# Kernel tuning notes

Measured on AMD Instinct MI355X. Metric: run time of the kernel, lower is better.

## Reference

```python
import jax, jax.numpy as jnp
import numpy as np

# e3nn normalize2mom constants: 1/sqrt(E[act(z)^2]) for z ~ N(0,1)
_z = np.random.default_rng(0).standard_normal(1_000_000)
_C_SILU = np.float32(1.0 / np.sqrt(np.mean((_z / (1.0 + np.exp(-_z))) ** 2)))
_C_SIGMOID = np.float32(1.0 / np.sqrt(np.mean((1.0 / (1.0 + np.exp(-_z))) ** 2)))

E = 131072
MUL0, MUL1 = 256, 128          # node irreps: 256x0e + 128x1e
RBF = 64
W_NUMEL = 256 + 256 + 128 + 128  # uvu weights in instruction order: A,C,B,D
INV_SQRT3 = np.float32(1.0 / np.sqrt(3.0))
INV_SQRT2 = np.float32(1.0 / np.sqrt(2.0))
INV_SQRT_FAN = np.float32(1.0 / np.sqrt(384.0))  # LinearRS rescale (fan_in=384)


def setup_inputs() -> dict:
    key = jax.random.key(0)
    ks = jax.random.split(key, 8)
    f32 = jnp.float32
    return {
        "node_input": jax.random.normal(ks[0], (E, MUL0 + MUL1 * 3), f32),
        "edge_attr": jax.random.normal(ks[1], (E, 4), f32),        # sh: 1x0e + 1x1e
        "edge_scalars": jax.random.normal(ks[2], (E, RBF), f32),
        "rad_w1": jax.random.normal(ks[3], (RBF, 64), f32) / np.float32(np.sqrt(RBF)),
        "rad_ln_g": jnp.ones((64,), f32),
        "rad_ln_b": jnp.zeros((64,), f32),
        "rad_w2": jax.random.normal(ks[4], (64, W_NUMEL), f32) / np.float32(8.0),
        "rad_offset": jnp.zeros((W_NUMEL,), f32),
        "lin_w0": jax.random.normal(ks[5], (384, 384), f32),
        "lin_b0": jnp.zeros((384,), f32),
        "lin_w1": jax.random.normal(ks[6], (384, MUL1), f32),
    }


def reference(node_input, edge_attr, edge_scalars, rad_w1, rad_ln_g, rad_ln_b,
              rad_w2, rad_offset, lin_w0, lin_b0, lin_w1):
    # --- RadialProfile: Linear(no bias) -> LayerNorm -> SiLU -> Linear(no bias) + offset
    h = edge_scalars @ rad_w1
    mu = jnp.mean(h, axis=-1, keepdims=True)
    var = jnp.var(h, axis=-1, keepdims=True)
    h = (h - mu) * jax.lax.rsqrt(var + 1e-5) * rad_ln_g + rad_ln_b
    h = jax.nn.silu(h)
    w = h @ rad_w2 + rad_offset                        # [E, 768] per-edge DTP weights
    wA, wC, wB, wD = w[:, :256], w[:, 256:512], w[:, 512:640], w[:, 640:]

    x0 = node_input[:, :MUL0]                          # [E,256]  0e
    x1 = node_input[:, MUL0:].reshape(-1, MUL1, 3)     # [E,128,3] 1e
    sh0 = edge_attr[:, 0:1]                            # [E,1]
    sh1 = edge_attr[:, 1:4]                            # [E,3]

    # --- DepthwiseTensorProduct ('uvu', path_weight = sqrt(dim(ir_out)), w3j orthonormal)
    outA = x0 * sh0 * wA                                                # 0e x 0e -> 0e [E,256]
    outB = jnp.einsum('eui,ei->eu', x1, sh1) * INV_SQRT3 * wB           # 1e . 1e -> 0e [E,128]
    outC = (x0 * wC)[:, :, None] * sh1[:, None, :]                      # 0e x 1e -> 1e [E,256,3]
    outD = jnp.cross(x1, sh1[:, None, :]) * INV_SQRT2 * wD[:, :, None]  # 1e x 1e -> 1e [E,128,3]

    d0 = jnp.concatenate([outA, outB], axis=-1)        # [E,384]   0e block (sorted irreps)
    d1 = jnp.concatenate([outC, outD], axis=1)         # [E,384,3] 1e block

    # --- LinearRS: per-irrep linear with 1/sqrt(fan_in) rescale; bias on 0e only
    out0 = d0 @ lin_w0 * INV_SQRT_FAN + lin_b0                       # [E,384] = 256 scalars + 128 gates
    out1 = jnp.einsum('eum,uv->evm', d1, lin_w1) * INV_SQRT_FAN      # [E,128,3] gated 1e

    # --- Gate: normalize2mom(SiLU) on scalars, normalize2mom(sigmoid) gates on 1e
    scalars = _C_SILU * jax.nn.silu(out0[:, :MUL0])
    gates = _C_SIGMOID * jax.nn.sigmoid(out0[:, MUL0:])
    gated = out1 * gates[:, :, None]
    return jnp.concatenate([scalars, gated.reshape(gated.shape[0], -1)], axis=-1)  # [E,640]
```

## Files before the change

### kernel.cpp

```cpp
#include <hip/hip_runtime.h>
#include <stdint.h>

typedef __attribute__((ext_vector_type(8))) short short8;
typedef __attribute__((ext_vector_type(4))) float f32x4;
typedef __attribute__((ext_vector_type(8))) float float8;

#define OW1R  0
#define OW2R  4096
#define OW0T  53248
#define OW1CT 200704
#define OW1DT 233472

#define OATTR 0
#define OES   512
#define OHS   4608
#define OD0   8704
#define OH    8704
#define OZC   33280
#define OZD0  49664
#define SMEM_BYTES 74240

static constexpr float C_SILU      = 1.6765390f;
static constexpr float C_SIG       = 1.8462240f;
static constexpr float INV_SQRT3   = 0.5773502691896258f;
static constexpr float INV_SQRT2   = 0.7071067811865476f;
static constexpr float INV_SQRT_FAN= 0.051031036307982884f;

__device__ __forceinline__ short f2bf(float f) {
  union { float f; uint32_t u; } v; v.f = f;
  uint32_t u = v.u;
  u += 0x7FFFu + ((u >> 16) & 1u);
  return (short)(u >> 16);
}

__device__ __forceinline__ f32x4 mfma16(short8 a, short8 b, f32x4 c) {
  return __builtin_amdgcn_mfma_f32_16x16x32_bf16(a, b, c, 0, 0, 0);
}

__device__ __forceinline__ short8 ldF(const short* __restrict__ W, int nkt, int nt, int kt, int lane) {
  return *(const short8*)(W + ((((nt * nkt) + kt) << 6) + lane) * 8);
}

__global__ void prep_weights(const float* __restrict__ rw1, const float* __restrict__ rw2,
                             const float* __restrict__ lw0, const float* __restrict__ lw1,
                             short* __restrict__ ws)
{
  int idx = blockIdx.x * blockDim.x + threadIdx.x;
  int stride = gridDim.x * blockDim.x;
  for (int i = idx; i < 4096; i += stride) {
    int e = i & 7, lane = (i >> 3) & 63, f = i >> 9;
    int kt = f & 1, nt = f >> 1;
    int n = nt * 16 + (lane & 15), k = kt * 32 + ((lane >> 4) << 3) + e;
    ws[OW1R + i] = f2bf(rw1[k * 64 + n]);
  }
  for (int i = idx; i < 49152; i += stride) {
    int e = i & 7, lane = (i >> 3) & 63, f = i >> 9;
    int kt = f & 1, nt = f >> 1;
    int n = nt * 16 + (lane & 15), k = kt * 32 + ((lane >> 4) << 3) + e;
    ws[OW2R + i] = f2bf(rw2[k * 768 + n]);
  }
  for (int i = idx; i < 147456; i += stride) {
    int e = i & 7, lane = (i >> 3) & 63, f = i >> 9;
    int kt = f % 12, nt = f / 12;
    int n = nt * 16 + (lane & 15), k = kt * 32 + ((lane >> 4) << 3) + e;
    ws[OW0T + i] = f2bf(lw0[k * 384 + n] * INV_SQRT_FAN);
  }
  for (int i = idx; i < 32768; i += stride) {
    int e = i & 7, lane = (i >> 3) & 63, f = i >> 9;
    int kt = f & 7, nt = f >> 3;
    int n = nt * 16 + (lane & 15), k = kt * 32 + ((lane >> 4) << 3) + e;
    ws[OW1CT + i] = f2bf(lw1[k * 128 + n] * INV_SQRT_FAN);
  }
  for (int i = idx; i < 16384; i += stride) {
    int e = i & 7, lane = (i >> 3) & 63, f = i >> 9;
    int kt = f & 3, nt = f >> 2;
    int n = nt * 16 + (lane & 15), k = kt * 32 + ((lane >> 4) << 3) + e;
    ws[OW1DT + i] = f2bf(lw1[(256 + k) * 128 + n] * INV_SQRT_FAN);
  }
}

#define SWZ(row, byte) ((byte) ^ ((((row) & 7) << 4) ^ (((row) & 8) << 2)))
#define LDA(base, c2, row, k0) \
  (*(const short8*)(smem + (base) + (row) * (c2) + SWZ(row, (k0) << 1)))
#define STBF(base, c2, row, col, val) \
  (*(short*)(smem + (base) + (row) * (c2) + SWZ(row, (col) << 1)) = f2bf(val))

__global__ __launch_bounds__(256) void fctp_fused(
    const float* __restrict__ node, const float* __restrict__ eattr,
    const float* __restrict__ escal, const float* __restrict__ lng,
    const float* __restrict__ lnb, const float* __restrict__ roff,
    const float* __restrict__ b0v, const short* __restrict__ ws,
    float* __restrict__ out)
{
  __shared__ char smem[SMEM_BYTES];
  const int t = threadIdx.x;
  const int lane = t & 63;
  const int w = t >> 6;
  const int row0 = blockIdx.x << 5;
  const int l15 = lane & 15;
  const int kof = (lane >> 4) << 3;
  const int rb0 = (lane >> 4) << 2;

  const int pr = t >> 3, pc0 = (t & 7) << 3;

  float4 lg0 = *(const float4*)(lng + pc0);
  float4 lg1 = *(const float4*)(lng + pc0 + 4);
  float4 lb0 = *(const float4*)(lnb + pc0);
  float4 lb1 = *(const float4*)(lnb + pc0 + 4);

  float offAr[4], offCr[4], offBr[2], offDr[2];
#pragma unroll
  for (int j = 0; j < 4; ++j) {
    int u = (((w << 2) + j) << 4) + l15;
    offAr[j] = roff[u];
    offCr[j] = roff[256 + u];
  }
#pragma unroll
  for (int j = 0; j < 2; ++j) {
    int u = (((w << 1) + j) << 4) + l15;
    offBr[j] = roff[512 + u];
    offDr[j] = roff[640 + u];
  }

  float s0r[2][4], sar[2][4], sbr[2][4], scr[2][4];
#pragma unroll
  for (int rt = 0; rt < 2; ++rt)
#pragma unroll
    for (int i = 0; i < 4; ++i) {
      int row = rt * 16 + rb0 + i;
      float4 att = *(const float4*)(eattr + (size_t)(row0 + row) * 4);
      s0r[rt][i] = att.x;
      sar[rt][i] = att.y;
      sbr[rt][i] = att.z;
      scr[rt][i] = att.w;
    }

  float x0r[4][2][4];
#pragma unroll
  for (int j = 0; j < 4; ++j) {
    int u = (((w << 2) + j) << 4) + l15;
#pragma unroll
    for (int rt = 0; rt < 2; ++rt)
#pragma unroll
      for (int i = 0; i < 4; ++i)
        x0r[j][rt][i] = node[(size_t)(row0 + rt * 16 + rb0 + i) * 640 + u];
  }
  float x1r[2][2][4][3];
#pragma unroll
  for (int j = 0; j < 2; ++j) {
    int u = (((w << 1) + j) << 4) + l15;
#pragma unroll
    for (int rt = 0; rt < 2; ++rt)
#pragma unroll
      for (int i = 0; i < 4; ++i) {
        const float* xp = node + (size_t)(row0 + rt * 16 + rb0 + i) * 640 + 256 + u * 3;
        x1r[j][rt][i][0] = xp[0];
        x1r[j][rt][i][1] = xp[1];
        x1r[j][rt][i][2] = xp[2];
      }
  }

  {
    short8 bf0 = ldF(ws + OW1R, 2, w, 0, lane);
    short8 bf1 = ldF(ws + OW1R, 2, w, 1, lane);
    float* sh_h = (float*)(smem + OH);
    int colh = (w << 4) + l15;
#pragma unroll
    for (int rt = 0; rt < 2; ++rt) {
      int r = rt * 16 + l15;
      const float* ep = escal + (size_t)(row0 + r) * 64;
      float8 e0 = *(const float8*)(ep + kof);
      float8 e1 = *(const float8*)(ep + 32 + kof);
      short8 ae0, ae1;
#pragma unroll
      for (int jj = 0; jj < 8; ++jj) { ae0[jj] = f2bf(e0[jj]); ae1[jj] = f2bf(e1[jj]); }
      f32x4 acc = {0.f, 0.f, 0.f, 0.f};
      acc = mfma16(ae0, bf0, acc);
      acc = mfma16(ae1, bf1, acc);
      int rb = rt * 16 + rb0;
#pragma unroll
      for (int i = 0; i < 4; ++i) sh_h[(rb + i) * 68 + colh] = acc[i];
    }
  }
  __syncthreads();

  {
    const float* sh_h = (const float*)(smem + OH);
    float vals[8]; float s = 0.f, s2 = 0.f;
#pragma unroll
    for (int j = 0; j < 8; ++j) {
      float v = sh_h[pr * 68 + pc0 + j];
      vals[j] = v; s += v; s2 += v * v;
    }
#pragma unroll
    for (int off = 1; off < 8; off <<= 1) {
      s  += __shfl_xor(s, off, 64);
      s2 += __shfl_xor(s2, off, 64);
    }
    float mu = s * 0.015625f;
    float var = s2 * 0.015625f - mu * mu;
    float rstd = rsqrtf(var + 1e-5f);
    float lg[8] = {lg0.x, lg0.y, lg0.z, lg0.w, lg1.x, lg1.y, lg1.z, lg1.w};
    float lb[8] = {lb0.x, lb0.y, lb0.z, lb0.w, lb1.x, lb1.y, lb1.z, lb1.w};
    short8 hv;
#pragma unroll
    for (int j = 0; j < 8; ++j) {
      float v = (vals[j] - mu) * rstd * lg[j] + lb[j];
      float sv = v / (1.f + __expf(-v));
      hv[j] = f2bf(sv);
    }
    *(short8*)(smem + OHS + pr * 128 + SWZ(pr, pc0 << 1)) = hv;
  }
  __syncthreads();

  {
    short8 a00 = LDA(OHS, 128, l15, kof);
    short8 a01 = LDA(OHS, 128, l15, 32 + kof);
    short8 a10 = LDA(OHS, 128, 16 + l15, kof);
    short8 a11 = LDA(OHS, 128, 16 + l15, 32 + kof);

#pragma unroll
    for (int j = 0; j < 4; ++j) {
      int ut = (w << 2) + j;
      short8 bA0 = ldF(ws + OW2R, 2, ut, 0, lane);
      short8 bA1 = ldF(ws + OW2R, 2, ut, 1, lane);
      short8 bC0 = ldF(ws + OW2R, 2, ut + 16, 0, lane);
      short8 bC1 = ldF(ws + OW2R, 2, ut + 16, 1, lane);
      int u = (ut << 4) + l15;
#pragma unroll
      for (int rt = 0; rt < 2; ++rt) {
        short8 fa = rt ? a10 : a00, fb = rt ? a11 : a01;
        f32x4 accA = {0.f,0.f,0.f,0.f}, accC = {0.f,0.f,0.f,0.f};
        accA = mfma16(fa, bA0, accA); accA = mfma16(fb, bA1, accA);
        accC = mfma16(fa, bC0, accC); accC = mfma16(fb, bC1, accC);
#pragma unroll
        for (int i = 0; i < 4; ++i) {
          int row = rt * 16 + rb0 + i;
          float x0v = x0r[j][rt][i];
          STBF(OD0, 768, row, u, x0v * s0r[rt][i] * (accA[i] + offAr[j]));
          STBF(OZC, 512, row, u, x0v * (accC[i] + offCr[j]));
        }
      }
    }
#pragma unroll
    for (int j = 0; j < 2; ++j) {
      int ut = (w << 1) + j;
      short8 bB0 = ldF(ws + OW2R, 2, 32 + ut, 0, lane);
      short8 bB1 = ldF(ws + OW2R, 2, 32 + ut, 1, lane);
      short8 bD0 = ldF(ws + OW2R, 2, 40 + ut, 0, lane);
      short8 bD1 = ldF(ws + OW2R, 2, 40 + ut, 1, lane);
      int u = (ut << 4) + l15;
#pragma unroll
      for (int rt = 0; rt < 2; ++rt) {
        short8 fa = rt ? a10 : a00, fb = rt ? a11 : a01;
        f32x4 accB = {0.f,0.f,0.f,0.f}, accD = {0.f,0.f,0.f,0.f};
        accB = mfma16(fa, bB0, accB); accB = mfma16(fb, bB1, accB);
        accD = mfma16(fa, bD0, accD); accD = mfma16(fb, bD1, accD);
#pragma unroll
        for (int i = 0; i < 4; ++i) {
          int row = rt * 16 + rb0 + i;
          float xa = x1r[j][rt][i][0], xb = x1r[j][rt][i][1], xc = x1r[j][rt][i][2];
          float sa = sar[rt][i], sb = sbr[rt][i], sc = scr[rt][i];
          float wB = accB[i] + offBr[j], wD = accD[i] + offDr[j];
          STBF(OD0, 768, row, 256 + u,
               (xa * sa + xb * sb + xc * sc) * INV_SQRT3 * wB);
          float zd = wD * INV_SQRT2;
          STBF(OZD0,          256, row, u, xa * zd);
          STBF(OZD0 + 8192,   256, row, u, xb * zd);
          STBF(OZD0 + 16384,  256, row, u, xc * zd);
        }
      }
    }
  }
  __syncthreads();


#pragma unroll
  for (int cp = 0; cp < 2; ++cp) {
    f32x4 sacc[2][2];
#pragma unroll
    for (int q = 0; q < 2; ++q)
#pragma unroll
      for (int rt = 0; rt < 2; ++rt) sacc[q][rt] = (f32x4){0.f, 0.f, 0.f, 0.f};
#pragma unroll
    for (int kt = 0; kt < 12; ++kt) {
      int k0 = kt * 32 + kof;
      short8 Af0 = LDA(OD0, 768, l15, k0);
      short8 Af1 = LDA(OD0, 768, 16 + l15, k0);
      short8 Bf0 = ldF(ws + OW0T, 12, (w << 2) + 2 * cp,     kt, lane);
      short8 Bf1 = ldF(ws + OW0T, 12, (w << 2) + 2 * cp + 1, kt, lane);
      sacc[0][0] = mfma16(Af0, Bf0, sacc[0][0]);
      sacc[0][1] = mfma16(Af1, Bf0, sacc[0][1]);
      sacc[1][0] = mfma16(Af0, Bf1, sacc[1][0]);
      sacc[1][1] = mfma16(Af1, Bf1, sacc[1][1]);
    }
#pragma unroll
    for (int q = 0; q < 2; ++q) {
      int col = (((w << 2) + 2 * cp + q) << 4) + l15;
      float bias = b0v[col];
#pragma unroll
      for (int rt = 0; rt < 2; ++rt) {
#pragma unroll
        for (int i = 0; i < 4; ++i) {
          float v = sacc[q][rt][i] + bias;
          float sv = v / (1.f + __expf(-v));
          out[(size_t)(row0 + rt * 16 + rb0 + i) * 640 + col] = C_SILU * sv;
        }
      }
    }
  }

  f32x4 gacc[2][2];
#pragma unroll
  for (int j = 0; j < 2; ++j)
#pragma unroll
    for (int rt = 0; rt < 2; ++rt) gacc[j][rt] = (f32x4){0.f, 0.f, 0.f, 0.f};
#pragma unroll
  for (int kt = 0; kt < 12; ++kt) {
    int k0 = kt * 32 + kof;
    short8 Af0 = LDA(OD0, 768, l15, k0);
    short8 Af1 = LDA(OD0, 768, 16 + l15, k0);
    short8 Bg0 = ldF(ws + OW0T, 12, 16 + (w << 1),     kt, lane);
    short8 Bg1 = ldF(ws + OW0T, 12, 16 + (w << 1) + 1, kt, lane);
    gacc[0][0] = mfma16(Af0, Bg0, gacc[0][0]);
    gacc[0][1] = mfma16(Af1, Bg0, gacc[0][1]);
    gacc[1][0] = mfma16(Af0, Bg1, gacc[1][0]);
    gacc[1][1] = mfma16(Af1, Bg1, gacc[1][1]);
  }

  f32x4 ycacc[2][2];
#pragma unroll
  for (int j = 0; j < 2; ++j)
#pragma unroll
    for (int rt = 0; rt < 2; ++rt) ycacc[j][rt] = (f32x4){0.f, 0.f, 0.f, 0.f};
  {
    short8 Az[2][8];
#pragma unroll
    for (int kt = 0; kt < 8; ++kt) {
      int k0 = kt * 32 + kof;
      Az[0][kt] = LDA(OZC, 512, l15, k0);
      Az[1][kt] = LDA(OZC, 512, 16 + l15, k0);
    }
#pragma unroll
    for (int j = 0; j < 2; ++j) {
      int vt = (w << 1) + j;
      short8 Bfr[8];
#pragma unroll
      for (int kt = 0; kt < 8; ++kt) Bfr[kt] = ldF(ws + OW1CT, 8, vt, kt, lane);
#pragma unroll
      for (int kt = 0; kt < 8; ++kt) {
        ycacc[j][0] = mfma16(Az[0][kt], Bfr[kt], ycacc[j][0]);
        ycacc[j][1] = mfma16(Az[1][kt], Bfr[kt], ycacc[j][1]);
      }
    }
  }

  f32x4 pacc[3][2][2];
#pragma unroll
  for (int m = 0; m < 3; ++m)
#pragma unroll
    for (int j = 0; j < 2; ++j)
#pragma unroll
      for (int rt = 0; rt < 2; ++rt) pacc[m][j][rt] = (f32x4){0.f, 0.f, 0.f, 0.f};
#pragma unroll
  for (int m = 0; m < 3; ++m) {
    short8 Az[2][4];
#pragma unroll
    for (int kt4 = 0; kt4 < 4; ++kt4) {
      int k0 = kt4 * 32 + kof;
      Az[0][kt4] = LDA(OZD0 + m * 8192, 256, l15, k0);
      Az[1][kt4] = LDA(OZD0 + m * 8192, 256, 16 + l15, k0);
    }
#pragma unroll
    for (int j = 0; j < 2; ++j) {
      int vt = (w << 1) + j;
      short8 Bfr[4];
#pragma unroll
      for (int kt4 = 0; kt4 < 4; ++kt4) Bfr[kt4] = ldF(ws + OW1DT, 4, vt, kt4, lane);
#pragma unroll
      for (int kt4 = 0; kt4 < 4; ++kt4) {
        pacc[m][j][0] = mfma16(Az[0][kt4], Bfr[kt4], pacc[m][j][0]);
        pacc[m][j][1] = mfma16(Az[1][kt4], Bfr[kt4], pacc[m][j][1]);
      }
    }
  }

  {
#pragma unroll
    for (int j = 0; j < 2; ++j) {
      int v = (((w << 1) + j) << 4) + l15;
      float bias = b0v[256 + v];
#pragma unroll
      for (int rt = 0; rt < 2; ++rt) {
#pragma unroll
        for (int i = 0; i < 4; ++i) {
          int row = rt * 16 + rb0 + i;
          float gate = C_SIG / (1.f + __expf(-(gacc[j][rt][i] + bias)));
          float ra = sar[rt][i], rb = sbr[rt][i], rc = scr[rt][i];
          float yc = ycacc[j][rt][i];
          float q0 = pacc[0][j][rt][i], q1 = pacc[1][j][rt][i], q2 = pacc[2][j][rt][i];
          float o0 = ra * yc + (rc * q1 - rb * q2);
          float o1 = rb * yc + (ra * q2 - rc * q0);
          float o2 = rc * yc + (rb * q0 - ra * q1);
          float* op = out + (size_t)(row0 + row) * 640 + 256 + v * 3;
          op[0] = o0 * gate; op[1] = o1 * gate; op[2] = o2 * gate;
        }
      }
    }
  }
}

extern "C" void kernel_launch(void* const* d_in, const int* in_sizes, int n_in,
                              void* d_out, int out_size, void* d_ws, size_t ws_size,
                              hipStream_t stream) {
  const float* node_input   = (const float*)d_in[0];
  const float* edge_attr    = (const float*)d_in[1];
  const float* edge_scalars = (const float*)d_in[2];
  const float* rad_w1       = (const float*)d_in[3];
  const float* rad_ln_g     = (const float*)d_in[4];
  const float* rad_ln_b     = (const float*)d_in[5];
  const float* rad_w2       = (const float*)d_in[6];
  const float* rad_offset   = (const float*)d_in[7];
  const float* lin_w0       = (const float*)d_in[8];
  const float* lin_b0       = (const float*)d_in[9];
  const float* lin_w1       = (const float*)d_in[10];
  short* wsb = (short*)d_ws;
  float* out = (float*)d_out;

  prep_weights<<<256, 256, 0, stream>>>(rad_w1, rad_w2, lin_w0, lin_w1, wsb);
  fctp_fused<<<131072 / 32, 256, 0, stream>>>(node_input, edge_attr, edge_scalars,
                                              rad_ln_g, rad_ln_b, rad_offset,
                                              lin_b0, wsb, out);
}
```

Measured before the change: 297.1 us.

## Split radial first layer and LayerNorm into a separate kernel

Moves the first radial linear layer, LayerNorm and SiLU out of the fused kernel into a new kernel that writes bf16 hidden activations to workspace. The main kernel then loads those activations straight from global memory into MFMA fragments. This drops two __syncthreads and the first-layer work from the main kernel, which may ease register pressure and shorten its critical path. The cost is an extra launch plus a round trip of roughly 16 MB of bf16 activations through global memory.

```diff
diff --git a/kernel.cpp b/kernel.cpp
--- a/kernel.cpp
+++ b/kernel.cpp
@@ -10,12 +10,9 @@
 #define OW0T  53248
 #define OW1CT 200704
 #define OW1DT 233472
-
-#define OATTR 0
-#define OES   512
-#define OHS   4608
+#define OHSG  249856
+
 #define OD0   8704
-#define OH    8704
 #define OZC   33280
 #define OZD0  49664
 #define SMEM_BYTES 74240
@@ -85,11 +82,81 @@
 #define STBF(base, c2, row, col, val) \
   (*(short*)(smem + (base) + (row) * (c2) + SWZ(row, (col) << 1)) = f2bf(val))
 
+__global__ __launch_bounds__(256) void hs_kernel(
+    const float* __restrict__ escal, const float* __restrict__ lng,
+    const float* __restrict__ lnb, const short* __restrict__ ws,
+    short* __restrict__ hsg)
+{
+  __shared__ float sh_h[32 * 68];
+  const int t = threadIdx.x;
+  const int lane = t & 63;
+  const int w = t >> 6;
+  const int row0 = blockIdx.x << 5;
+  const int l15 = lane & 15;
+  const int kof = (lane >> 4) << 3;
+  const int rb0 = (lane >> 4) << 2;
+  const int pr = t >> 3, pc0 = (t & 7) << 3;
+
+  float4 lg0 = *(const float4*)(lng + pc0);
+  float4 lg1 = *(const float4*)(lng + pc0 + 4);
+  float4 lb0 = *(const float4*)(lnb + pc0);
+  float4 lb1 = *(const float4*)(lnb + pc0 + 4);
+
+  {
+    short8 bf0 = ldF(ws + OW1R, 2, w, 0, lane);
+    short8 bf1 = ldF(ws + OW1R, 2, w, 1, lane);
+    int colh = (w << 4) + l15;
+#pragma unroll
+    for (int rt = 0; rt < 2; ++rt) {
+      int r = rt * 16 + l15;
+      const float* ep = escal + (size_t)(row0 + r) * 64;
+      float8 e0 = *(const float8*)(ep + kof);
+      float8 e1 = *(const float8*)(ep + 32 + kof);
+      short8 ae0, ae1;
+#pragma unroll
+      for (int jj = 0; jj < 8; ++jj) { ae0[jj] = f2bf(e0[jj]); ae1[jj] = f2bf(e1[jj]); }
+      f32x4 acc = {0.f, 0.f, 0.f, 0.f};
+      acc = mfma16(ae0, bf0, acc);
+      acc = mfma16(ae1, bf1, acc);
+      int rb = rt * 16 + rb0;
+#pragma unroll
+      for (int i = 0; i < 4; ++i) sh_h[(rb + i) * 68 + colh] = acc[i];
+    }
+  }
+  __syncthreads();
+
+  {
+    float vals[8]; float s = 0.f, s2 = 0.f;
+#pragma unroll
+    for (int j = 0; j < 8; ++j) {
+      float v = sh_h[pr * 68 + pc0 + j];
+      vals[j] = v; s += v; s2 += v * v;
+    }
+#pragma unroll
+    for (int off = 1; off < 8; off <<= 1) {
+      s  += __shfl_xor(s, off, 64);
+      s2 += __shfl_xor(s2, off, 64);
+    }
+    float mu = s * 0.015625f;
+    float var = s2 * 0.015625f - mu * mu;
+    float rstd = rsqrtf(var + 1e-5f);
+    float lg[8] = {lg0.x, lg0.y, lg0.z, lg0.w, lg1.x, lg1.y, lg1.z, lg1.w};
+    float lb[8] = {lb0.x, lb0.y, lb0.z, lb0.w, lb1.x, lb1.y, lb1.z, lb1.w};
+    short8 hv;
+#pragma unroll
+    for (int j = 0; j < 8; ++j) {
+      float v = (vals[j] - mu) * rstd * lg[j] + lb[j];
+      float sv = v / (1.f + __expf(-v));
+      hv[j] = f2bf(sv);
+    }
+    *(short8*)(hsg + (size_t)(row0 + pr) * 64 + pc0) = hv;
+  }
+}
+
 __global__ __launch_bounds__(256) void fctp_fused(
     const float* __restrict__ node, const float* __restrict__ eattr,
-    const float* __restrict__ escal, const float* __restrict__ lng,
-    const float* __restrict__ lnb, const float* __restrict__ roff,
-    const float* __restrict__ b0v, const short* __restrict__ ws,
+    const float* __restrict__ roff, const float* __restrict__ b0v,
+    const short* __restrict__ ws, const short* __restrict__ hsg,
     float* __restrict__ out)
 {
   __shared__ char smem[SMEM_BYTES];
@@ -101,13 +168,6 @@
   const int kof = (lane >> 4) << 3;
   const int rb0 = (lane >> 4) << 2;
 
-  const int pr = t >> 3, pc0 = (t & 7) << 3;
-
-  float4 lg0 = *(const float4*)(lng + pc0);
-  float4 lg1 = *(const float4*)(lng + pc0 + 4);
-  float4 lb0 = *(const float4*)(lnb + pc0);
-  float4 lb1 = *(const float4*)(lnb + pc0 + 4);
-
   float offAr[4], offCr[4], offBr[2], offDr[2];
 #pragma unroll
   for (int j = 0; j < 4; ++j) {
@@ -160,65 +220,12 @@
       }
   }
 
+  short8 a00 = *(const short8*)(hsg + (size_t)(row0 + l15) * 64 + kof);
+  short8 a01 = *(const short8*)(hsg + (size_t)(row0 + l15) * 64 + 32 + kof);
+  short8 a10 = *(const short8*)(hsg + (size_t)(row0 + 16 + l15) * 64 + kof);
+  short8 a11 = *(const short8*)(hsg + (size_t)(row0 + 16 + l15) * 64 + 32 + kof);
+
   {
-    short8 bf0 = ldF(ws + OW1R, 2, w, 0, lane);
-    short8 bf1 = ldF(ws + OW1R, 2, w, 1, lane);
-    float* sh_h = (float*)(smem + OH);
-    int colh = (w << 4) + l15;
-#pragma unroll
-    for (int rt = 0; rt < 2; ++rt) {
-      int r = rt * 16 + l15;
-      const float* ep = escal + (size_t)(row0 + r) * 64;
-      float8 e0 = *(const float8*)(ep + kof);
-      float8 e1 = *(const float8*)(ep + 32 + kof);
-      short8 ae0, ae1;
-#pragma unroll
-      for (int jj = 0; jj < 8; ++jj) { ae0[jj] = f2bf(e0[jj]); ae1[jj] = f2bf(e1[jj]); }
-      f32x4 acc = {0.f, 0.f, 0.f, 0.f};
-      acc = mfma16(ae0, bf0, acc);
-      acc = mfma16(ae1, bf1, acc);
-      int rb = rt * 16 + rb0;
-#pragma unroll
-      for (int i = 0; i < 4; ++i) sh_h[(rb + i) * 68 + colh] = acc[i];
-    }
-  }
-  __syncthreads();
-
-  {
-    const float* sh_h = (const float*)(smem + OH);
-    float vals[8]; float s = 0.f, s2 = 0.f;
-#pragma unroll
-    for (int j = 0; j < 8; ++j) {
-      float v = sh_h[pr * 68 + pc0 + j];
-      vals[j] = v; s += v; s2 += v * v;
-    }
-#pragma unroll
-    for (int off = 1; off < 8; off <<= 1) {
-      s  += __shfl_xor(s, off, 64);
-      s2 += __shfl_xor(s2, off, 64);
-    }
-    float mu = s * 0.015625f;
-    float var = s2 * 0.015625f - mu * mu;
-    float rstd = rsqrtf(var + 1e-5f);
-    float lg[8] = {lg0.x, lg0.y, lg0.z, lg0.w, lg1.x, lg1.y, lg1.z, lg1.w};
-    float lb[8] = {lb0.x, lb0.y, lb0.z, lb0.w, lb1.x, lb1.y, lb1.z, lb1.w};
-    short8 hv;
-#pragma unroll
-    for (int j = 0; j < 8; ++j) {
-      float v = (vals[j] - mu) * rstd * lg[j] + lb[j];
-      float sv = v / (1.f + __expf(-v));
-      hv[j] = f2bf(sv);
-    }
-    *(short8*)(smem + OHS + pr * 128 + SWZ(pr, pc0 << 1)) = hv;
-  }
-  __syncthreads();
-
-  {
-    short8 a00 = LDA(OHS, 128, l15, kof);
-    short8 a01 = LDA(OHS, 128, l15, 32 + kof);
-    short8 a10 = LDA(OHS, 128, 16 + l15, kof);
-    short8 a11 = LDA(OHS, 128, 16 + l15, 32 + kof);
-
 #pragma unroll
     for (int j = 0; j < 4; ++j) {
       int ut = (w << 2) + j;
@@ -428,7 +435,8 @@
   float* out = (float*)d_out;
 
   prep_weights<<<256, 256, 0, stream>>>(rad_w1, rad_w2, lin_w0, lin_w1, wsb);
-  fctp_fused<<<131072 / 32, 256, 0, stream>>>(node_input, edge_attr, edge_scalars,
-                                              rad_ln_g, rad_ln_b, rad_offset,
-                                              lin_b0, wsb, out);
-}
+  hs_kernel<<<131072 / 32, 256, 0, stream>>>(edge_scalars, rad_ln_g, rad_ln_b,
+                                             wsb, wsb + OHSG);
+  fctp_fused<<<131072 / 32, 256, 0, stream>>>(node_input, edge_attr, rad_offset,
+                                              lin_b0, wsb, wsb + OHSG, out);
+}
```

Result: slower. 304.9 us (+2.6%).
